# Kernel optimization log

Measured on AMD Instinct MI355X. Metric: run time of the kernel, lower is better.

## Reference

```python
import jax, jax.numpy as jnp
import numpy as np

N = 2_000_000
C = 128
B = 50_000


def setup_inputs() -> dict:
    key = jax.random.key(0)
    k1, k2, k3 = jax.random.split(key, 3)
    x = jax.random.normal(k1, (N, C), dtype=jnp.float32)
    weight_c = jax.random.normal(k2, (C, C), dtype=jnp.float32) * (1.0 / np.sqrt(C))
    batch = jnp.sort(jax.random.randint(k3, (N,), 0, B, dtype=jnp.int64))
    return {"x": x, "weight_c": weight_c, "batch": batch, "num_segments": B}


def reference(x, weight_c, batch, num_segments):
    # global_mean_pool: segment sum / count (count clamped to >=1)
    sums = jax.ops.segment_sum(x, batch, num_segments=num_segments)          # [B, C]
    ones = jnp.ones((x.shape[0], 1), dtype=x.dtype)
    counts = jax.ops.segment_sum(ones, batch, num_segments=num_segments)    # [B, 1]
    c = sums / jnp.maximum(counts, 1.0)
    # context transform
    c = jnp.tanh(c @ weight_c)                                              # [B, C]
    # gather context back to nodes
    c_nodes = c[batch]                                                      # [N, C]
    # sigmoid gate on per-node dot product, then global_add_pool
    gate = jax.nn.sigmoid(jnp.sum(x * c_nodes, axis=1, keepdims=True))      # [N, 1]
    h = jax.ops.segment_sum(gate * x, batch, num_segments=num_segments)     # [B, C]
    return h
```

## Files before the change

kernel.cpp:

```cpp
#include <hip/hip_runtime.h>
#include <math.h>

#define C        128
#define BLK      256
#define WPB      (BLK / 64)
#define MAXSLOT  12
#define NROW     (4 * MAXSLOT)
#define WSTRIDE  68

__device__ __forceinline__ float4 f4add(float4 a, float4 b) {
    float4 r; r.x = a.x + b.x; r.y = a.y + b.y; r.z = a.z + b.z; r.w = a.w + b.w; return r;
}
__device__ __forceinline__ float4 f4shfl_xor(float4 v, int m) {
    float4 r;
    r.x = __shfl_xor(v.x, m, 64);
    r.y = __shfl_xor(v.y, m, 64);
    r.z = __shfl_xor(v.z, m, 64);
    r.w = __shfl_xor(v.w, m, 64);
    return r;
}
__device__ __forceinline__ float4 f4mask(float4 v, bool keep) {
    v.x = keep ? v.x : 0.f; v.y = keep ? v.y : 0.f;
    v.z = keep ? v.z : 0.f; v.w = keep ? v.w : 0.f;
    return v;
}
__device__ __forceinline__ float fast_tanh(float v) {
    const float t = __expf(2.0f * v);
    return 1.0f - 2.0f / (t + 1.0f);
}
__device__ __forceinline__ float fast_sigmoid(float v) {
    return 1.0f / (1.0f + __expf(-v));
}
__device__ __forceinline__ uint32_t pack2(float a, float b) {
    uint32_t ua = __float_as_uint(a), ub = __float_as_uint(b);
    ua = (ua + 0x7FFFu + ((ua >> 16) & 1u)) >> 16;
    ub = (ub + 0x7FFFu + ((ub >> 16) & 1u)) & 0xFFFF0000u;
    return ua | ub;
}
__device__ __forceinline__ float4 unpack4(uint32_t a, uint32_t b) {
    float4 v;
    v.x = __uint_as_float(a << 16);
    v.y = __uint_as_float(a & 0xFFFF0000u);
    v.z = __uint_as_float(b << 16);
    v.w = __uint_as_float(b & 0xFFFF0000u);
    return v;
}
__device__ __forceinline__ float row16_sum(float d) {
    d += __int_as_float(__builtin_amdgcn_update_dpp(0, __float_as_int(d), 0x128, 0xF, 0xF, true));
    d += __int_as_float(__builtin_amdgcn_update_dpp(0, __float_as_int(d), 0x124, 0xF, 0xF, true));
    d += __int_as_float(__builtin_amdgcn_update_dpp(0, __float_as_int(d), 0x122, 0xF, 0xF, true));
    d += __int_as_float(__builtin_amdgcn_update_dpp(0, __float_as_int(d), 0x121, 0xF, 0xF, true));
    return d;
}
__device__ __forceinline__ float dot8(float4 lo, float4 hi, float4 clo, float4 chi) {
    float a = lo.x * clo.x + lo.y * clo.y;
    float b = lo.z * clo.z + lo.w * clo.w;
    float c = hi.x * chi.x + hi.y * chi.y;
    float d = hi.z * chi.z + hi.w * chi.w;
    return (a + b) + (c + d);
}

extern "C" __global__ __launch_bounds__(BLK)
__attribute__((amdgpu_waves_per_eu(2, 2)))
void cba_dense2_kernel(const float* __restrict__ x,
                       const float* __restrict__ W,
                       const int* __restrict__ batch,
                       float* __restrict__ out,
                       int N, int B, int totalWaves)
{
    __shared__ uint32_t sWb[C * WSTRIDE];
    __shared__ float4   sMean[WPB * 32];

    const int t    = threadIdx.x;
    const int lane = t & 63;
    const int wid  = t >> 6;
    const int rg   = lane >> 4;
    const int c16  = lane & 15;

    const float2* W2 = (const float2*)W;
    for (int p = t; p < C * 64; p += BLK) {
        const int k = p >> 6, j = p & 63;
        const int rot = (k >> 5) << 3;
        const int pos = (j < 32) ? ((j + rot) & 31)
                                 : (32 + ((j - 32 + rot) & 31));
        const float2 wv = W2[p];
        sWb[k * WSTRIDE + pos] = pack2(wv.x, wv.y);
    }
    __syncthreads();

    const int gw = blockIdx.x * WPB + wid;

    const int qn = B / totalWaves;
    const int r  = B % totalWaves;
    const int segStart = gw * qn + (gw < r ? gw : r);
    const int myCnt    = qn + (gw < r ? 1 : 0);

    const int tl     = lane < myCnt ? lane : myCnt;
    const int target = segStart + tl;
    int lo_ = 0, hi_ = N;
    while (lo_ < hi_) {
        int mid = (lo_ + hi_) >> 1;
        if (batch[mid] < target) lo_ = mid + 1; else hi_ = mid;
    }
    const int bs = lo_;

    const float4* x4  = (const float4*)x;
    const int     Nm1 = N - 1;
    float4* mb = sMean + wid * 32;
    const int wco = (2 * c16 + (rg << 3)) & 31;

    float4 pl[MAXSLOT], ph[MAXSLOT];

#define ISSUE(sseg, eseg)                                              \
    {                                                                  \
        int lastv = (eseg) - 1;                                        \
        lastv = lastv > (sseg) ? lastv : (sseg);                       \
        lastv = lastv < Nm1 ? lastv : Nm1;                             \
        _Pragma("unroll")                                              \
        for (int sl = 0; sl < MAXSLOT; ++sl) {                         \
            const int row = (sseg) + 4 * sl + rg;                      \
            const int rc  = row < (eseg) ? row : lastv;                \
            pl[sl] = x4[(size_t)rc * 32 + c16];                        \
            ph[sl] = x4[(size_t)rc * 32 + 16 + c16];                   \
        }                                                              \
    }

    int sCur = 0, eCur = 0;
    if (myCnt > 0) {
        sCur = __shfl(bs, 0, 64);
        eCur = __shfl(bs, 1, 64);
        ISSUE(sCur, eCur);
    }

    for (int k = 0; k < myCnt; ++k) {
        const int b   = segStart + k;
        const int s   = sCur;
        const int e   = eCur;
        const int cnt = e - s;

        uint4 rbPk[MAXSLOT];
        float4 alo = make_float4(0.f,0.f,0.f,0.f), ahi = alo;
#pragma unroll
        for (int sl = 0; sl < MAXSLOT; ++sl) {
            const bool valid = (s + 4 * sl + rg) < e;
            const float4 lo = f4mask(pl[sl], valid);
            const float4 hi = f4mask(ph[sl], valid);
            alo = f4add(alo, lo); ahi = f4add(ahi, hi);
            rbPk[sl].x = pack2(lo.x, lo.y); rbPk[sl].y = pack2(lo.z, lo.w);
            rbPk[sl].z = pack2(hi.x, hi.y); rbPk[sl].w = pack2(hi.z, hi.w);
        }
        for (int i = s + NROW + rg; i < e; i += 4) {
            alo = f4add(alo, x4[(size_t)i * 32 + c16]);
            ahi = f4add(ahi, x4[(size_t)i * 32 + 16 + c16]);
        }

        if (k + 1 < myCnt) {
            sCur = __shfl(bs, k + 1, 64);
            eCur = __shfl(bs, k + 2, 64);
            ISSUE(sCur, eCur);
        }
        __builtin_amdgcn_sched_barrier(0);

        alo = f4add(alo, f4shfl_xor(alo, 16));
        alo = f4add(alo, f4shfl_xor(alo, 32));
        ahi = f4add(ahi, f4shfl_xor(ahi, 16));
        ahi = f4add(ahi, f4shfl_xor(ahi, 32));
        const float inv = 1.0f / (float)(cnt > 0 ? cnt : 1);
        if (lane < 16) {
            float4 mlo, mhi;
            mlo.x = alo.x*inv; mlo.y = alo.y*inv; mlo.z = alo.z*inv; mlo.w = alo.w*inv;
            mhi.x = ahi.x*inv; mhi.y = ahi.y*inv; mhi.z = ahi.z*inv; mhi.w = ahi.w*inv;
            mb[c16]      = mlo;
            mb[16 + c16] = mhi;
        }

        float4 plo = make_float4(0.f,0.f,0.f,0.f), phi = plo;
#pragma unroll
        for (int jq = 0; jq < 8; ++jq) {
            const float4 m4 = mb[(rg << 3) + jq];
            const int kb = (rg << 5) + (jq << 2);
#define FMAK(mm, kk)                                                           \
            {                                                                  \
                const uint32_t* rowp = &sWb[(kk) * WSTRIDE];                   \
                const uint2 ul = *(const uint2*)&rowp[wco];                    \
                const uint2 uh = *(const uint2*)&rowp[32 + wco];               \
                plo.x = fmaf(mm, __uint_as_float(ul.x << 16),         plo.x);  \
                plo.y = fmaf(mm, __uint_as_float(ul.x & 0xFFFF0000u), plo.y);  \
                plo.z = fmaf(mm, __uint_as_float(ul.y << 16),         plo.z);  \
                plo.w = fmaf(mm, __uint_as_float(ul.y & 0xFFFF0000u), plo.w);  \
                phi.x = fmaf(mm, __uint_as_float(uh.x << 16),         phi.x);  \
                phi.y = fmaf(mm, __uint_as_float(uh.x & 0xFFFF0000u), phi.y);  \
                phi.z = fmaf(mm, __uint_as_float(uh.y << 16),         phi.z);  \
                phi.w = fmaf(mm, __uint_as_float(uh.y & 0xFFFF0000u), phi.w);  \
            }
            FMAK(m4.x, kb + 0); FMAK(m4.y, kb + 1);
            FMAK(m4.z, kb + 2); FMAK(m4.w, kb + 3);
#undef FMAK
        }
        plo = f4add(plo, f4shfl_xor(plo, 16));
        plo = f4add(plo, f4shfl_xor(plo, 32));
        phi = f4add(phi, f4shfl_xor(phi, 16));
        phi = f4add(phi, f4shfl_xor(phi, 32));
        float4 clo, chi;
        clo.x = fast_tanh(plo.x); clo.y = fast_tanh(plo.y);
        clo.z = fast_tanh(plo.z); clo.w = fast_tanh(plo.w);
        chi.x = fast_tanh(phi.x); chi.y = fast_tanh(phi.y);
        chi.z = fast_tanh(phi.z); chi.w = fast_tanh(phi.w);

        float4 hlo = make_float4(0.f,0.f,0.f,0.f), hhi = hlo;
#pragma unroll
        for (int sl = 0; sl < MAXSLOT; ++sl) {
            const float4 lo = unpack4(rbPk[sl].x, rbPk[sl].y);
            const float4 hi = unpack4(rbPk[sl].z, rbPk[sl].w);
            float d = dot8(lo, hi, clo, chi);
            d = row16_sum(d);
            const float g = fast_sigmoid(d);
            hlo.x = fmaf(g, lo.x, hlo.x); hlo.y = fmaf(g, lo.y, hlo.y);
            hlo.z = fmaf(g, lo.z, hlo.z); hlo.w = fmaf(g, lo.w, hlo.w);
            hhi.x = fmaf(g, hi.x, hhi.x); hhi.y = fmaf(g, hi.y, hhi.y);
            hhi.z = fmaf(g, hi.z, hhi.z); hhi.w = fmaf(g, hi.w, hhi.w);
        }
        for (int i = s + NROW + rg; i < e; i += 4) {
            const float4 lo = x4[(size_t)i * 32 + c16];
            const float4 hi = x4[(size_t)i * 32 + 16 + c16];
            float d = dot8(lo, hi, clo, chi);
            d = row16_sum(d);
            const float g = fast_sigmoid(d);
            hlo.x = fmaf(g, lo.x, hlo.x); hlo.y = fmaf(g, lo.y, hlo.y);
            hlo.z = fmaf(g, lo.z, hlo.z); hlo.w = fmaf(g, lo.w, hlo.w);
            hhi.x = fmaf(g, hi.x, hhi.x); hhi.y = fmaf(g, hi.y, hhi.y);
            hhi.z = fmaf(g, hi.z, hhi.z); hhi.w = fmaf(g, hi.w, hhi.w);
        }
        hlo = f4add(hlo, f4shfl_xor(hlo, 16));
        hlo = f4add(hlo, f4shfl_xor(hlo, 32));
        hhi = f4add(hhi, f4shfl_xor(hhi, 16));
        hhi = f4add(hhi, f4shfl_xor(hhi, 32));
        if (lane < 16) {
            ((float4*)out)[(size_t)b * 32 + c16]      = hlo;
            ((float4*)out)[(size_t)b * 32 + 16 + c16] = hhi;
        }
    }
#undef ISSUE
}

extern "C" void kernel_launch(void* const* d_in, const int* in_sizes, int n_in,
                              void* d_out, int out_size, void* d_ws, size_t ws_size,
                              hipStream_t stream) {
    const float* x     = (const float*)d_in[0];
    const float* W     = (const float*)d_in[1];
    const int*   batch = (const int*)d_in[2];
    float*       out   = (float*)d_out;

    const int N = in_sizes[0] / C;
    const int B = out_size / C;

    const int grid       = 512;
    const int totalWaves = grid * WPB;
    hipLaunchKernelGGL(cba_dense2_kernel, dim3(grid), dim3(BLK), 0, stream,
                       x, W, batch, out, N, B, totalWaves);
}
```

Before: 243.3 us.

## Switch to 32-lane row layout and interleave segments across block waves

Each wave now reads a full 128-float row with 32 lanes holding one float4 each, two rows per load slot, where before 16 lanes handled a row with two float4 loads. MAXSLOT doubles so the same 48 rows are prefetched. Segments are assigned per block and interleaved across its four waves, and the dot product uses an extra ds_swizzle xor-16 step to sum across the full row. The aim is fewer load instructions per row, cheaper cross-lane reductions and better load balance, at the cost of an extra swizzle per row and more per-slot packing work.

```diff
diff --git a/kernel.cpp b/kernel.cpp
--- a/kernel.cpp
+++ b/kernel.cpp
@@ -4,8 +4,8 @@
 #define C        128
 #define BLK      256
 #define WPB      (BLK / 64)
-#define MAXSLOT  12
-#define NROW     (4 * MAXSLOT)
+#define MAXSLOT  24
+#define NROW     (2 * MAXSLOT)
 #define WSTRIDE  68
 
 __device__ __forceinline__ float4 f4add(float4 a, float4 b) {
@@ -37,6 +37,9 @@
     ub = (ub + 0x7FFFu + ((ub >> 16) & 1u)) & 0xFFFF0000u;
     return ua | ub;
 }
+__device__ __forceinline__ uint2 packf4(float4 v) {
+    uint2 r; r.x = pack2(v.x, v.y); r.y = pack2(v.z, v.w); return r;
+}
 __device__ __forceinline__ float4 unpack4(uint32_t a, uint32_t b) {
     float4 v;
     v.x = __uint_as_float(a << 16);
@@ -52,21 +55,17 @@
     d += __int_as_float(__builtin_amdgcn_update_dpp(0, __float_as_int(d), 0x121, 0xF, 0xF, true));
     return d;
 }
-__device__ __forceinline__ float dot8(float4 lo, float4 hi, float4 clo, float4 chi) {
-    float a = lo.x * clo.x + lo.y * clo.y;
-    float b = lo.z * clo.z + lo.w * clo.w;
-    float c = hi.x * chi.x + hi.y * chi.y;
-    float d = hi.z * chi.z + hi.w * chi.w;
-    return (a + b) + (c + d);
+__device__ __forceinline__ float xor16_add(float d) {
+    return d + __int_as_float(__builtin_amdgcn_ds_swizzle(__float_as_int(d), 0x401F));
 }
 
 extern "C" __global__ __launch_bounds__(BLK)
 __attribute__((amdgpu_waves_per_eu(2, 2)))
-void cba_dense2_kernel(const float* __restrict__ x,
-                       const float* __restrict__ W,
-                       const int* __restrict__ batch,
-                       float* __restrict__ out,
-                       int N, int B, int totalWaves)
+void cba_densefull_kernel(const float* __restrict__ x,
+                          const float* __restrict__ W,
+                          const int* __restrict__ batch,
+                          float* __restrict__ out,
+                          int N, int B, int nBlocks)
 {
     __shared__ uint32_t sWb[C * WSTRIDE];
     __shared__ float4   sMean[WPB * 32];
@@ -74,6 +73,8 @@
     const int t    = threadIdx.x;
     const int lane = t & 63;
     const int wid  = t >> 6;
+    const int sr   = lane >> 5;
+    const int q5   = lane & 31;
     const int rg   = lane >> 4;
     const int c16  = lane & 15;
 
@@ -88,19 +89,20 @@
     }
     __syncthreads();
 
-    const int gw = blockIdx.x * WPB + wid;
-
-    const int qn = B / totalWaves;
-    const int r  = B % totalWaves;
-    const int segStart = gw * qn + (gw < r ? gw : r);
-    const int myCnt    = qn + (gw < r ? 1 : 0);
-
-    const int tl     = lane < myCnt ? lane : myCnt;
-    const int target = segStart + tl;
+    const int bid = blockIdx.x;
+    const int qb  = B / nBlocks;
+    const int rb  = B % nBlocks;
+    const int blockStart = bid * qb + (bid < rb ? bid : rb);
+    const int blkCnt     = qb + (bid < rb ? 1 : 0);
+    const int myCnt      = (blkCnt > wid) ? ((blkCnt - wid + 3) >> 2) : 0;
+
+    const int l   = lane & 31;
+    int tgt = blockStart + 4 * l + wid + ((lane >> 5) & 1);
+    tgt = tgt < B ? tgt : B;
     int lo_ = 0, hi_ = N;
     while (lo_ < hi_) {
         int mid = (lo_ + hi_) >> 1;
-        if (batch[mid] < target) lo_ = mid + 1; else hi_ = mid;
+        if (batch[mid] < tgt) lo_ = mid + 1; else hi_ = mid;
     }
     const int bs = lo_;
 
@@ -109,7 +111,7 @@
     float4* mb = sMean + wid * 32;
     const int wco = (2 * c16 + (rg << 3)) & 31;
 
-    float4 pl[MAXSLOT], ph[MAXSLOT];
+    float4 pv[MAXSLOT];
 
 #define ISSUE(sseg, eseg)                                              \
     {                                                                  \
@@ -118,60 +120,51 @@
         lastv = lastv < Nm1 ? lastv : Nm1;                             \
         _Pragma("unroll")                                              \
         for (int sl = 0; sl < MAXSLOT; ++sl) {                         \
-            const int row = (sseg) + 4 * sl + rg;                      \
+            const int row = (sseg) + 2 * sl + sr;                      \
             const int rc  = row < (eseg) ? row : lastv;                \
-            pl[sl] = x4[(size_t)rc * 32 + c16];                        \
-            ph[sl] = x4[(size_t)rc * 32 + 16 + c16];                   \
+            pv[sl] = x4[(size_t)rc * 32 + q5];                         \
         }                                                              \
     }
 
     int sCur = 0, eCur = 0;
     if (myCnt > 0) {
         sCur = __shfl(bs, 0, 64);
-        eCur = __shfl(bs, 1, 64);
+        eCur = __shfl(bs, 32, 64);
         ISSUE(sCur, eCur);
     }
 
     for (int k = 0; k < myCnt; ++k) {
-        const int b   = segStart + k;
+        const int b   = blockStart + 4 * k + wid;
         const int s   = sCur;
         const int e   = eCur;
         const int cnt = e - s;
 
-        uint4 rbPk[MAXSLOT];
-        float4 alo = make_float4(0.f,0.f,0.f,0.f), ahi = alo;
+        uint2 rbPk[MAXSLOT];
+        float4 acc = make_float4(0.f, 0.f, 0.f, 0.f);
 #pragma unroll
         for (int sl = 0; sl < MAXSLOT; ++sl) {
-            const bool valid = (s + 4 * sl + rg) < e;
-            const float4 lo = f4mask(pl[sl], valid);
-            const float4 hi = f4mask(ph[sl], valid);
-            alo = f4add(alo, lo); ahi = f4add(ahi, hi);
-            rbPk[sl].x = pack2(lo.x, lo.y); rbPk[sl].y = pack2(lo.z, lo.w);
-            rbPk[sl].z = pack2(hi.x, hi.y); rbPk[sl].w = pack2(hi.z, hi.w);
-        }
-        for (int i = s + NROW + rg; i < e; i += 4) {
-            alo = f4add(alo, x4[(size_t)i * 32 + c16]);
-            ahi = f4add(ahi, x4[(size_t)i * 32 + 16 + c16]);
-        }
+            const bool valid = (s + 2 * sl + sr) < e;
+            const float4 v = f4mask(pv[sl], valid);
+            acc = f4add(acc, v);
+            rbPk[sl] = packf4(v);
+        }
+        for (int i = s + NROW + sr; i < e; i += 2)
+            acc = f4add(acc, x4[(size_t)i * 32 + q5]);
 
         if (k + 1 < myCnt) {
             sCur = __shfl(bs, k + 1, 64);
-            eCur = __shfl(bs, k + 2, 64);
+            eCur = __shfl(bs, 32 + k + 1, 64);
             ISSUE(sCur, eCur);
         }
         __builtin_amdgcn_sched_barrier(0);
 
-        alo = f4add(alo, f4shfl_xor(alo, 16));
-        alo = f4add(alo, f4shfl_xor(alo, 32));
-        ahi = f4add(ahi, f4shfl_xor(ahi, 16));
-        ahi = f4add(ahi, f4shfl_xor(ahi, 32));
+        acc = f4add(acc, f4shfl_xor(acc, 32));
         const float inv = 1.0f / (float)(cnt > 0 ? cnt : 1);
-        if (lane < 16) {
-            float4 mlo, mhi;
-            mlo.x = alo.x*inv; mlo.y = alo.y*inv; mlo.z = alo.z*inv; mlo.w = alo.w*inv;
-            mhi.x = ahi.x*inv; mhi.y = ahi.y*inv; mhi.z = ahi.z*inv; mhi.w = ahi.w*inv;
-            mb[c16]      = mlo;
-            mb[16 + c16] = mhi;
+        if (lane < 32) {
+            float4 m4;
+            m4.x = acc.x * inv; m4.y = acc.y * inv;
+            m4.z = acc.z * inv; m4.w = acc.w * inv;
+            mb[q5] = m4;
         }
 
         float4 plo = make_float4(0.f,0.f,0.f,0.f), phi = plo;
@@ -201,44 +194,37 @@
         plo = f4add(plo, f4shfl_xor(plo, 32));
         phi = f4add(phi, f4shfl_xor(phi, 16));
         phi = f4add(phi, f4shfl_xor(phi, 32));
-        float4 clo, chi;
-        clo.x = fast_tanh(plo.x); clo.y = fast_tanh(plo.y);
-        clo.z = fast_tanh(plo.z); clo.w = fast_tanh(plo.w);
-        chi.x = fast_tanh(phi.x); chi.y = fast_tanh(phi.y);
-        chi.z = fast_tanh(phi.z); chi.w = fast_tanh(phi.w);
-
-        float4 hlo = make_float4(0.f,0.f,0.f,0.f), hhi = hlo;
+        float4 cv;
+        {
+            const float4 csel = (lane & 16) ?
+                make_float4(fast_tanh(phi.x), fast_tanh(phi.y), fast_tanh(phi.z), fast_tanh(phi.w)) :
+                make_float4(fast_tanh(plo.x), fast_tanh(plo.y), fast_tanh(plo.z), fast_tanh(plo.w));
+            cv = csel;
+        }
+
+        float4 hacc = make_float4(0.f, 0.f, 0.f, 0.f);
 #pragma unroll
         for (int sl = 0; sl < MAXSLOT; ++sl) {
-            const float4 lo = unpack4(rbPk[sl].x, rbPk[sl].y);
-            const float4 hi = unpack4(rbPk[sl].z, rbPk[sl].w);
-            float d = dot8(lo, hi, clo, chi);
+            const float4 v = unpack4(rbPk[sl].x, rbPk[sl].y);
+            float d = v.x * cv.x + v.y * cv.y + v.z * cv.z + v.w * cv.w;
             d = row16_sum(d);
+            d = xor16_add(d);
             const float g = fast_sigmoid(d);
-            hlo.x = fmaf(g, lo.x, hlo.x); hlo.y = fmaf(g, lo.y, hlo.y);
-            hlo.z = fmaf(g, lo.z, hlo.z); hlo.w = fmaf(g, lo.w, hlo.w);
-            hhi.x = fmaf(g, hi.x, hhi.x); hhi.y = fmaf(g, hi.y, hhi.y);
-            hhi.z = fmaf(g, hi.z, hhi.z); hhi.w = fmaf(g, hi.w, hhi.w);
-        }
-        for (int i = s + NROW + rg; i < e; i += 4) {
-            const float4 lo = x4[(size_t)i * 32 + c16];
-            const float4 hi = x4[(size_t)i * 32 + 16 + c16];
-            float d = dot8(lo, hi, clo, chi);
+            hacc.x = fmaf(g, v.x, hacc.x); hacc.y = fmaf(g, v.y, hacc.y);
+            hacc.z = fmaf(g, v.z, hacc.z); hacc.w = fmaf(g, v.w, hacc.w);
+        }
+        for (int i = s + NROW + sr; i < e; i += 2) {
+            const float4 v = x4[(size_t)i * 32 + q5];
+            float d = v.x * cv.x + v.y * cv.y + v.z * cv.z + v.w * cv.w;
             d = row16_sum(d);
+            d = xor16_add(d);
             const float g = fast_sigmoid(d);
-            hlo.x = fmaf(g, lo.x, hlo.x); hlo.y = fmaf(g, lo.y, hlo.y);
-            hlo.z = fmaf(g, lo.z, hlo.z); hlo.w = fmaf(g, lo.w, hlo.w);
-            hhi.x = fmaf(g, hi.x, hhi.x); hhi.y = fmaf(g, hi.y, hhi.y);
-            hhi.z = fmaf(g, hi.z, hhi.z); hhi.w = fmaf(g, hi.w, hhi.w);
-        }
-        hlo = f4add(hlo, f4shfl_xor(hlo, 16));
-        hlo = f4add(hlo, f4shfl_xor(hlo, 32));
-        hhi = f4add(hhi, f4shfl_xor(hhi, 16));
-        hhi = f4add(hhi, f4shfl_xor(hhi, 32));
-        if (lane < 16) {
-            ((float4*)out)[(size_t)b * 32 + c16]      = hlo;
-            ((float4*)out)[(size_t)b * 32 + 16 + c16] = hhi;
-        }
+            hacc.x = fmaf(g, v.x, hacc.x); hacc.y = fmaf(g, v.y, hacc.y);
+            hacc.z = fmaf(g, v.z, hacc.z); hacc.w = fmaf(g, v.w, hacc.w);
+        }
+        hacc = f4add(hacc, f4shfl_xor(hacc, 32));
+        if (lane < 32)
+            ((float4*)out)[(size_t)b * 32 + q5] = hacc;
     }
 #undef ISSUE
 }
@@ -254,8 +240,7 @@
     const int N = in_sizes[0] / C;
     const int B = out_size / C;
 
-    const int grid       = 512;
-    const int totalWaves = grid * WPB;
-    hipLaunchKernelGGL(cba_dense2_kernel, dim3(grid), dim3(BLK), 0, stream,
-                       x, W, batch, out, N, B, totalWaves);
-}
+    const int grid = 512;
+    hipLaunchKernelGGL(cba_densefull_kernel, dim3(grid), dim3(BLK), 0, stream,
+                       x, W, batch, out, N, B, grid);
+}
```

Measured after the change: 255.4 us. 1.05x slower.
